# Kernel tuning notes

Measured on AMD Instinct MI355X. Metric: run time of the kernel, lower is better.

The kernel has to match this reference:

```python
import jax, jax.numpy as jnp
import numpy as np

B, S, E, D = 8, 2048, 512, 512  # batch, seq (mesh edges), elem_size, embd_size


def setup_inputs() -> dict:
    key = jax.random.key(0)
    ks = jax.random.split(key, 5)
    scale = 1.0 / np.sqrt(E)
    return {
        "x": jax.random.normal(ks[0], (B, S, E), dtype=jnp.float32),
        "Wq": jax.random.normal(ks[1], (E, D), dtype=jnp.float32) * scale,
        "bq": jax.random.normal(ks[2], (D,), dtype=jnp.float32) * 0.01,
        "Wk": jax.random.normal(ks[3], (E, D), dtype=jnp.float32) * scale,
        "bk": jax.random.normal(ks[4], (D,), dtype=jnp.float32) * 0.01,
    }


def reference(x, Wq, bq, Wk, bk):
    elem_size = x.shape[-1]
    q = jax.nn.relu(x @ Wq + bq)              # [B,S,D]
    k = jax.nn.relu(x @ Wk + bk)              # [B,S,D]
    scores = jnp.einsum("bqd,bkd->bqk", q, k) / (elem_size ** 0.5)  # [B,S,S]
    # nn.Softmax(dim=1): normalize over the QUERY axis (column-wise softmax)
    attn = jax.nn.softmax(scores, axis=1)
    new_values = jnp.einsum("bqk,bke->bqe", attn, x)  # V = raw x (use_V=False)
    return x + new_values                     # residual connection
```

## Files before the change

### kernel.cpp

```cpp
#include <hip/hip_runtime.h>
#include <hip/hip_bf16.h>
#include <math.h>

#define Bb 8
#define Ss 2048
#define Ee 512
#define Dd 512
#define QSPLIT 16

typedef __bf16 bf16x8 __attribute__((ext_vector_type(8)));
typedef __bf16 bf16x4 __attribute__((ext_vector_type(4)));
typedef float f32x4 __attribute__((ext_vector_type(4)));


__device__ __forceinline__ void stage64(ushort* lds, const __bf16* gbase,
                                        int ldg, int wave, int lane) {
#pragma unroll
    for (int t = 0; t < 4; ++t) {
        const int slot = wave * 256 + t * 64 + lane;
        const int row  = slot >> 3;
        const int c    = (slot & 7) ^ (row & 7);
        __builtin_amdgcn_global_load_lds(
            (const __attribute__((address_space(1))) void*)(gbase + (size_t)row * ldg + c * 8),
            (__attribute__((address_space(3))) void*)(lds + (size_t)slot * 8),
            16, 0, 0);
    }
}

__device__ __forceinline__ void stage64h(ushort* lds, const __bf16* gbase,
                                         int ldg, int wave, int lane) {
#pragma unroll
    for (int t = 0; t < 2; ++t) {
        const int slot = wave * 128 + t * 64 + lane;
        const int row  = slot >> 3;
        const int c    = (slot & 7) ^ (row & 7);
        __builtin_amdgcn_global_load_lds(
            (const __attribute__((address_space(1))) void*)(gbase + (size_t)row * ldg + c * 8),
            (__attribute__((address_space(3))) void*)(lds + (size_t)slot * 8),
            16, 0, 0);
    }
}

__global__ __launch_bounds__(256) void prep_x(const float* __restrict__ in,
                                              __bf16* __restrict__ xb,
                                              __bf16* __restrict__ xT) {
    __shared__ float tile[64][65];
    const int b  = blockIdx.z;
    const int e0 = blockIdx.x * 64;
    const int s0 = blockIdx.y * 64;
    const float* ip = in + (size_t)b * Ss * Ee;
    __bf16* xbp = xb + (size_t)b * Ss * Ee;
    __bf16* xTp = xT + (size_t)b * Ee * Ss;
    const int tid  = threadIdx.x;
    const int rrow = tid >> 4;
    const int c4   = (tid & 15) * 4;
    #pragma unroll
    for (int it = 0; it < 4; ++it) {
        const int r = it * 16 + rrow;
        const float4 v = *(const float4*)&ip[(size_t)(s0 + r) * Ee + e0 + c4];
        bf16x4 h;
        h[0] = (__bf16)v.x; h[1] = (__bf16)v.y; h[2] = (__bf16)v.z; h[3] = (__bf16)v.w;
        *(bf16x4*)&xbp[(size_t)(s0 + r) * Ee + e0 + c4] = h;
        tile[r][c4 + 0] = v.x; tile[r][c4 + 1] = v.y;
        tile[r][c4 + 2] = v.z; tile[r][c4 + 3] = v.w;
    }
    __syncthreads();
    const int sc  = (tid & 7) * 8;
    const int erb = tid >> 3;
    #pragma unroll
    for (int it = 0; it < 2; ++it) {
        const int er = it * 32 + erb;
        bf16x8 o;
        #pragma unroll
        for (int t = 0; t < 8; ++t) o[t] = (__bf16)tile[sc + t][er];
        *(bf16x8*)&xTp[(size_t)(e0 + er) * Ss + s0 + sc] = o;
    }
}

__global__ void transpose_w(const float* __restrict__ Wq, const float* __restrict__ Wk,
                            __bf16* __restrict__ WqT, __bf16* __restrict__ WkT) {
    __shared__ float tile[32][33];
    const float* in = blockIdx.z ? Wk : Wq;
    __bf16* out = blockIdx.z ? WkT : WqT;
    const int x0 = blockIdx.x * 32;
    const int y0 = blockIdx.y * 32;
    for (int i = threadIdx.y; i < 32; i += 8)
        tile[i][threadIdx.x] = in[(size_t)(y0 + i) * 512 + (x0 + threadIdx.x)];
    __syncthreads();
    for (int i = threadIdx.y; i < 32; i += 8)
        out[(size_t)(x0 + i) * 512 + (y0 + threadIdx.x)] = (__bf16)tile[threadIdx.x][i];
}

__global__ __launch_bounds__(256, 4) void proj_kernel(
    const __bf16* __restrict__ X,
    const __bf16* __restrict__ WqT, const __bf16* __restrict__ WkT,
    const float* __restrict__ bq, const float* __restrict__ bk,
    __bf16* __restrict__ qb, __bf16* __restrict__ kb)
{
    __shared__ __align__(16) ushort smem[2 * 128 * 64];
    ushort* As = smem;
    ushort* Bs = smem + 128 * 64;
    const __bf16* WT  = blockIdx.z ? WkT : WqT;
    const float* bias = blockIdx.z ? bk : bq;
    __bf16* Out       = blockIdx.z ? kb : qb;

    const int tid = threadIdx.x;
    const int wave = tid >> 6, lane = tid & 63, quad = lane >> 4, l16 = lane & 15;
    const int wm = (wave >> 1) * 64, wn = (wave & 1) * 64;
    const int m0 = blockIdx.y * 128, n0 = blockIdx.x * 128;
    const int K = 512;
    const int sw0 = ((quad)     ^ (l16 & 7)) * 8;
    const int sw1 = ((quad + 4) ^ (l16 & 7)) * 8;

    f32x4 acc[4][4];
    f32x4 zero = {0.f, 0.f, 0.f, 0.f};
    for (int i = 0; i < 4; i++) for (int j = 0; j < 4; j++) acc[i][j] = zero;

    for (int k0 = 0; k0 < K; k0 += 64) {
        stage64(As, X  + (size_t)m0 * K + k0, K, wave, lane);
        stage64(Bs, WT + (size_t)n0 * K + k0, K, wave, lane);
        __syncthreads();
        #pragma unroll
        for (int h = 0; h < 2; h++) {
            const int sw = h ? sw1 : sw0;
            bf16x8 af[4], bfr[4];
            for (int i = 0; i < 4; i++) af[i]  = *(bf16x8*)&As[(wm + i * 16 + l16) * 64 + sw];
            for (int j = 0; j < 4; j++) bfr[j] = *(bf16x8*)&Bs[(wn + j * 16 + l16) * 64 + sw];
            for (int i = 0; i < 4; i++)
                for (int j = 0; j < 4; j++)
                    acc[i][j] = __builtin_amdgcn_mfma_f32_16x16x32_bf16(af[i], bfr[j], acc[i][j], 0, 0, 0);
        }
        __syncthreads();
    }

    ushort* patch = smem + wave * 4096;
    for (int j = 0; j < 4; j++) {
        const float bv = bias[n0 + wn + j * 16 + l16];
        const int colsw = (j * 16 + l16) ^ (quad * 16);
        for (int i = 0; i < 4; i++)
            for (int rr = 0; rr < 4; rr++) {
                float v = acc[i][j][rr] + bv;
                v = v > 0.f ? v : 0.f;
                patch[(i * 16 + quad * 4 + rr) * 64 + colsw] = ((ushort2*)&v)[0].y;
            }
    }
    __syncthreads();
    #pragma unroll
    for (int it = 0; it < 8; it++) {
        const int lr = it * 8 + (lane >> 3);
        const int lc = ((lane & 7) * 8) ^ (((lr >> 2) & 3) * 16);
        const bf16x8 v = *(const bf16x8*)&patch[lr * 64 + lc];
        *(bf16x8*)&Out[(size_t)(m0 + wm + lr) * 512 + n0 + wn + (((lane & 7) * 8))] = v;
    }
}

__global__ __launch_bounds__(256, 4) void scores_kernel(
    const __bf16* __restrict__ Q,
    const __bf16* __restrict__ Km,
    __bf16* __restrict__ P,
    float* __restrict__ Lp)
{
    __shared__ __align__(16) ushort smem[2 * 128 * 64];
    __shared__ float stats[256];
    ushort* As = smem;
    ushort* Bs = smem + 128 * 64;
    const int id = blockIdx.x;
    const int b = id & 7;
    const int rest = id >> 3;
    const int qy = rest >> 4;
    const int m0 = qy * 128;
    const int n0 = (rest & 15) * 128;
    const __bf16* A  = Q  + (size_t)b * Ss * Dd;
    const __bf16* Bp = Km + (size_t)b * Ss * Dd;
    __bf16* C = P + (size_t)b * Ss * Ss;

    const int tid = threadIdx.x;
    const int wave = tid >> 6, lane = tid & 63, quad = lane >> 4, l16 = lane & 15;
    const int wm = (wave >> 1) * 64, wn = (wave & 1) * 64;
    const int sw0 = ((quad)     ^ (l16 & 7)) * 8;
    const int sw1 = ((quad + 4) ^ (l16 & 7)) * 8;
    const float scale = 0.044194173824159216f;
    const float SHIFT = 8.0f;

    f32x4 acc[4][4];
    f32x4 zero = {0.f, 0.f, 0.f, 0.f};
    for (int i = 0; i < 4; i++) for (int j = 0; j < 4; j++) acc[i][j] = zero;

    for (int k0 = 0; k0 < Dd; k0 += 64) {
        stage64(As, A  + (size_t)m0 * Dd + k0, Dd, wave, lane);
        stage64(Bs, Bp + (size_t)n0 * Dd + k0, Dd, wave, lane);
        __syncthreads();
        #pragma unroll
        for (int h = 0; h < 2; h++) {
            const int sw = h ? sw1 : sw0;
            bf16x8 af[4], bfr[4];
            for (int i = 0; i < 4; i++) af[i]  = *(bf16x8*)&As[(wm + i * 16 + l16) * 64 + sw];
            for (int j = 0; j < 4; j++) bfr[j] = *(bf16x8*)&Bs[(wn + j * 16 + l16) * 64 + sw];
            for (int i = 0; i < 4; i++)
                for (int j = 0; j < 4; j++)
                    acc[i][j] = __builtin_amdgcn_mfma_f32_16x16x32_bf16(af[i], bfr[j], acc[i][j], 0, 0, 0);
        }
        __syncthreads();
    }

    float* Ls = stats;
    const int half = wave >> 1;
    ushort* patch = smem + wave * 4096;
    float lj[4];
    for (int j = 0; j < 4; j++) {
        float l = 0.f;
        const int colsw = (j * 16 + l16) ^ (quad * 16);
        for (int i = 0; i < 4; i++)
            for (int rr = 0; rr < 4; rr++) {
                const float e = __expf(fmaf(acc[i][j][rr], scale, -SHIFT));
                const __bf16 pb = (__bf16)e;
                patch[(i * 16 + quad * 4 + rr) * 64 + colsw] = *(const ushort*)&pb;
                l += e;
            }
        l += __shfl_xor(l, 16);
        l += __shfl_xor(l, 32);
        lj[j] = l;
    }
    if (quad == 0)
        for (int j = 0; j < 4; j++) Ls[half * 128 + wn + j * 16 + l16] = lj[j];
    __syncthreads();
    if (tid < 128) {
        const size_t o = ((size_t)qy * Bb + b) * Ss + n0 + tid;
        Lp[o] = Ls[tid] + Ls[128 + tid];
    }
    #pragma unroll
    for (int it = 0; it < 8; it++) {
        const int lr = it * 8 + (lane >> 3);
        const int lc = ((lane & 7) * 8) ^ (((lr >> 2) & 3) * 16);
        const bf16x8 v = *(const bf16x8*)&patch[lr * 64 + lc];
        *(bf16x8*)&C[(size_t)(m0 + wm + lr) * Ss + n0 + wn + ((lane & 7) * 8)] = v;
    }
}

__global__ void stats_combine(const float* __restrict__ Lp, float* __restrict__ Cinv) {
    const int idx = blockIdx.x * 256 + threadIdx.x;
    float l = 0.f;
    for (int qy = 0; qy < QSPLIT; qy++) l += Lp[(size_t)qy * Bb * Ss + idx];
    Cinv[idx] = 1.0f / l;
}

__global__ void xscale_kernel(const __bf16* __restrict__ xT,
                              const float* __restrict__ Cinv,
                              __bf16* __restrict__ XC) {
    const int r = blockIdx.x;
    const int b = r >> 9;
    const size_t base = (size_t)r * Ss;
    const float* cp = Cinv + (size_t)b * Ss;
    const int k0 = threadIdx.x * 8;
    const bf16x8 v = *(const bf16x8*)&xT[base + k0];
    const float4 c0 = *(const float4*)&cp[k0];
    const float4 c1 = *(const float4*)&cp[k0 + 4];
    bf16x8 o;
    o[0] = (__bf16)((float)v[0] * c0.x);
    o[1] = (__bf16)((float)v[1] * c0.y);
    o[2] = (__bf16)((float)v[2] * c0.z);
    o[3] = (__bf16)((float)v[3] * c0.w);
    o[4] = (__bf16)((float)v[4] * c1.x);
    o[5] = (__bf16)((float)v[5] * c1.y);
    o[6] = (__bf16)((float)v[6] * c1.z);
    o[7] = (__bf16)((float)v[7] * c1.w);
    *(bf16x8*)&XC[base + k0] = o;
}

__global__ __launch_bounds__(256, 4) void pv_kernel(
    const __bf16* __restrict__ P,
    const __bf16* __restrict__ XC,
    const __bf16* __restrict__ XB,
    float* __restrict__ Out)
{
    __shared__ __align__(16) ushort smem[64 * 64 + 128 * 64];
    ushort* As = smem;
    ushort* Bs = smem + 64 * 64;
    const int id = blockIdx.x;
    const int b = id & 7;
    const int rest = id >> 3;
    const int m0 = (rest >> 2) * 64;
    const int n0 = (rest & 3) * 128;
    const __bf16* A  = P  + (size_t)b * Ss * Ss;
    const __bf16* Bp = XC + (size_t)b * Ee * Ss;

    const int tid = threadIdx.x;
    const int wave = tid >> 6, lane = tid & 63, quad = lane >> 4, l16 = lane & 15;
    const int wm = (wave >> 1) * 32, wn = (wave & 1) * 64;
    const int sw0 = ((quad)     ^ (l16 & 7)) * 8;
    const int sw1 = ((quad + 4) ^ (l16 & 7)) * 8;

    f32x4 acc[2][4];
    f32x4 zero = {0.f, 0.f, 0.f, 0.f};
    for (int i = 0; i < 2; i++) for (int j = 0; j < 4; j++) acc[i][j] = zero;

    for (int k0 = 0; k0 < Ss; k0 += 64) {
        stage64h(As, A  + (size_t)m0 * Ss + k0, Ss, wave, lane);
        stage64 (Bs, Bp + (size_t)n0 * Ss + k0, Ss, wave, lane);
        __syncthreads();
        #pragma unroll
        for (int h = 0; h < 2; h++) {
            const int sw = h ? sw1 : sw0;
            bf16x8 af[2], bfr[4];
            for (int i = 0; i < 2; i++) af[i]  = *(bf16x8*)&As[(wm + i * 16 + l16) * 64 + sw];
            for (int j = 0; j < 4; j++) bfr[j] = *(bf16x8*)&Bs[(wn + j * 16 + l16) * 64 + sw];
            for (int i = 0; i < 2; i++)
                for (int j = 0; j < 4; j++)
                    acc[i][j] = __builtin_amdgcn_mfma_f32_16x16x32_bf16(af[i], bfr[j], acc[i][j], 0, 0, 0);
        }
        __syncthreads();
    }

    for (int i = 0; i < 2; i++) {
        for (int j = 0; j < 4; j++) {
            const int col = n0 + wn + j * 16 + l16;
            for (int rr = 0; rr < 4; rr++) {
                const int row = m0 + wm + i * 16 + quad * 4 + rr;
                const size_t idx = ((size_t)b * Ss + row) * Ee + col;
                Out[idx] = (float)XB[idx] + acc[i][j][rr];
            }
        }
    }
}

extern "C" void kernel_launch(void* const* d_in, const int* in_sizes, int n_in,
                              void* d_out, int out_size, void* d_ws, size_t ws_size,
                              hipStream_t stream) {
    const float* x  = (const float*)d_in[0];
    const float* Wq = (const float*)d_in[1];
    const float* bq = (const float*)d_in[2];
    const float* Wk = (const float*)d_in[3];
    const float* bk = (const float*)d_in[4];
    float* out = (float*)d_out;

    char* ws = (char*)d_ws;
    size_t off = 0;
    auto alloc = [&](size_t bytes) -> void* {
        void* p = ws + off;
        off += (bytes + 255) & ~(size_t)255;
        return p;
    };
    __bf16* P    = (__bf16*)alloc((size_t)Bb * Ss * Ss * 2);
    __bf16* xb   = (__bf16*)alloc((size_t)Bb * Ss * Ee * 2);
    __bf16* qb   = (__bf16*)alloc((size_t)Bb * Ss * Dd * 2);
    __bf16* kb   = (__bf16*)alloc((size_t)Bb * Ss * Dd * 2);
    __bf16* xT   = (__bf16*)alloc((size_t)Bb * Ee * Ss * 2);
    __bf16* WqT  = (__bf16*)alloc((size_t)512 * 512 * 2);
    __bf16* WkT  = (__bf16*)alloc((size_t)512 * 512 * 2);
    float*  Lp   = (float*)alloc((size_t)QSPLIT * Bb * Ss * 4);
    float*  Cinv = (float*)alloc((size_t)Bb * Ss * 4);
    if (off > ws_size) return;
    __bf16* XC = qb;

    prep_x<<<dim3(8, 32, 8), 256, 0, stream>>>(x, xb, xT);
    transpose_w<<<dim3(16, 16, 2), dim3(32, 8), 0, stream>>>(Wq, Wk, WqT, WkT);

    proj_kernel<<<dim3(4, 128, 2), 256, 0, stream>>>(xb, WqT, WkT, bq, bk, qb, kb);

    scores_kernel<<<dim3(2048), 256, 0, stream>>>(qb, kb, P, Lp);
    stats_combine<<<dim3(Bb * Ss / 256), 256, 0, stream>>>(Lp, Cinv);

    xscale_kernel<<<dim3(Bb * Ee), 256, 0, stream>>>(xT, Cinv, XC);

    pv_kernel<<<dim3(1024), 256, 0, stream>>>(P, XC, xb, out);
}
```

Before: 221.7 us.

## Double-buffer LDS staging in proj, scores and pv GEMM kernels

Adds ping-pong LDS buffers to the three GEMM main loops. The next K-tile is prefetched with global_load_lds while the current one feeds the MFMAs, using explicit vmcnt waits and raw s_barrier in place of __syncthreads. The aim is to hide global-memory latency behind compute. In exchange, LDS per block doubles (64 KB for proj/scores), which may lower occupancy below the launch_bounds target of 4 blocks, and the hand-tuned vmcnt counts must match the number of loads each stage issues.

```diff
diff --git a/kernel.cpp b/kernel.cpp
--- a/kernel.cpp
+++ b/kernel.cpp
@@ -97,9 +97,11 @@
     const float* __restrict__ bq, const float* __restrict__ bk,
     __bf16* __restrict__ qb, __bf16* __restrict__ kb)
 {
-    __shared__ __align__(16) ushort smem[2 * 128 * 64];
-    ushort* As = smem;
-    ushort* Bs = smem + 128 * 64;
+    __shared__ __align__(16) ushort smem[4 * 128 * 64];
+    ushort* As0 = smem;
+    ushort* Bs0 = smem + 8192;
+    ushort* As1 = smem + 16384;
+    ushort* Bs1 = smem + 24576;
     const __bf16* WT  = blockIdx.z ? WkT : WqT;
     const float* bias = blockIdx.z ? bk : bq;
     __bf16* Out       = blockIdx.z ? kb : qb;
@@ -116,21 +118,35 @@
     f32x4 zero = {0.f, 0.f, 0.f, 0.f};
     for (int i = 0; i < 4; i++) for (int j = 0; j < 4; j++) acc[i][j] = zero;
 
-    for (int k0 = 0; k0 < K; k0 += 64) {
-        stage64(As, X  + (size_t)m0 * K + k0, K, wave, lane);
-        stage64(Bs, WT + (size_t)n0 * K + k0, K, wave, lane);
-        __syncthreads();
+    stage64(As0, X  + (size_t)m0 * K, K, wave, lane);
+    stage64(Bs0, WT + (size_t)n0 * K, K, wave, lane);
+    #pragma unroll
+    for (int t = 0; t < 8; ++t) {
+        ushort* Ac = (t & 1) ? As1 : As0;
+        ushort* Bc = (t & 1) ? Bs1 : Bs0;
+        if (t < 7) {
+            ushort* An = (t & 1) ? As0 : As1;
+            ushort* Bn = (t & 1) ? Bs0 : Bs1;
+            const int kn = (t + 1) * 64;
+            stage64(An, X  + (size_t)m0 * K + kn, K, wave, lane);
+            stage64(Bn, WT + (size_t)n0 * K + kn, K, wave, lane);
+            asm volatile("s_waitcnt vmcnt(8)" ::: "memory");
+        } else {
+            asm volatile("s_waitcnt vmcnt(0)" ::: "memory");
+        }
+        __builtin_amdgcn_s_barrier();
         #pragma unroll
         for (int h = 0; h < 2; h++) {
             const int sw = h ? sw1 : sw0;
             bf16x8 af[4], bfr[4];
-            for (int i = 0; i < 4; i++) af[i]  = *(bf16x8*)&As[(wm + i * 16 + l16) * 64 + sw];
-            for (int j = 0; j < 4; j++) bfr[j] = *(bf16x8*)&Bs[(wn + j * 16 + l16) * 64 + sw];
+            for (int i = 0; i < 4; i++) af[i]  = *(bf16x8*)&Ac[(wm + i * 16 + l16) * 64 + sw];
+            for (int j = 0; j < 4; j++) bfr[j] = *(bf16x8*)&Bc[(wn + j * 16 + l16) * 64 + sw];
             for (int i = 0; i < 4; i++)
                 for (int j = 0; j < 4; j++)
                     acc[i][j] = __builtin_amdgcn_mfma_f32_16x16x32_bf16(af[i], bfr[j], acc[i][j], 0, 0, 0);
         }
-        __syncthreads();
+        __builtin_amdgcn_sched_barrier(0);
+        __builtin_amdgcn_s_barrier();
     }
 
     ushort* patch = smem + wave * 4096;
@@ -160,10 +176,12 @@
     __bf16* __restrict__ P,
     float* __restrict__ Lp)
 {
-    __shared__ __align__(16) ushort smem[2 * 128 * 64];
+    __shared__ __align__(16) ushort smem[4 * 128 * 64];
     __shared__ float stats[256];
-    ushort* As = smem;
-    ushort* Bs = smem + 128 * 64;
+    ushort* As0 = smem;
+    ushort* Bs0 = smem + 8192;
+    ushort* As1 = smem + 16384;
+    ushort* Bs1 = smem + 24576;
     const int id = blockIdx.x;
     const int b = id & 7;
     const int rest = id >> 3;
@@ -186,21 +204,35 @@
     f32x4 zero = {0.f, 0.f, 0.f, 0.f};
     for (int i = 0; i < 4; i++) for (int j = 0; j < 4; j++) acc[i][j] = zero;
 
-    for (int k0 = 0; k0 < Dd; k0 += 64) {
-        stage64(As, A  + (size_t)m0 * Dd + k0, Dd, wave, lane);
-        stage64(Bs, Bp + (size_t)n0 * Dd + k0, Dd, wave, lane);
-        __syncthreads();
+    stage64(As0, A  + (size_t)m0 * Dd, Dd, wave, lane);
+    stage64(Bs0, Bp + (size_t)n0 * Dd, Dd, wave, lane);
+    #pragma unroll
+    for (int t = 0; t < 8; ++t) {
+        ushort* Ac = (t & 1) ? As1 : As0;
+        ushort* Bc = (t & 1) ? Bs1 : Bs0;
+        if (t < 7) {
+            ushort* An = (t & 1) ? As0 : As1;
+            ushort* Bn = (t & 1) ? Bs0 : Bs1;
+            const int kn = (t + 1) * 64;
+            stage64(An, A  + (size_t)m0 * Dd + kn, Dd, wave, lane);
+            stage64(Bn, Bp + (size_t)n0 * Dd + kn, Dd, wave, lane);
+            asm volatile("s_waitcnt vmcnt(8)" ::: "memory");
+        } else {
+            asm volatile("s_waitcnt vmcnt(0)" ::: "memory");
+        }
+        __builtin_amdgcn_s_barrier();
         #pragma unroll
         for (int h = 0; h < 2; h++) {
             const int sw = h ? sw1 : sw0;
             bf16x8 af[4], bfr[4];
-            for (int i = 0; i < 4; i++) af[i]  = *(bf16x8*)&As[(wm + i * 16 + l16) * 64 + sw];
-            for (int j = 0; j < 4; j++) bfr[j] = *(bf16x8*)&Bs[(wn + j * 16 + l16) * 64 + sw];
+            for (int i = 0; i < 4; i++) af[i]  = *(bf16x8*)&Ac[(wm + i * 16 + l16) * 64 + sw];
+            for (int j = 0; j < 4; j++) bfr[j] = *(bf16x8*)&Bc[(wn + j * 16 + l16) * 64 + sw];
             for (int i = 0; i < 4; i++)
                 for (int j = 0; j < 4; j++)
                     acc[i][j] = __builtin_amdgcn_mfma_f32_16x16x32_bf16(af[i], bfr[j], acc[i][j], 0, 0, 0);
         }
-        __syncthreads();
+        __builtin_amdgcn_sched_barrier(0);
+        __builtin_amdgcn_s_barrier();
     }
 
     float* Ls = stats;
@@ -273,9 +305,11 @@
     const __bf16* __restrict__ XB,
     float* __restrict__ Out)
 {
-    __shared__ __align__(16) ushort smem[64 * 64 + 128 * 64];
-    ushort* As = smem;
-    ushort* Bs = smem + 64 * 64;
+    __shared__ __align__(16) ushort smem[2 * (64 * 64 + 128 * 64)];
+    ushort* As0 = smem;
+    ushort* Bs0 = smem + 4096;
+    ushort* As1 = smem + 12288;
+    ushort* Bs1 = smem + 16384;
     const int id = blockIdx.x;
     const int b = id & 7;
     const int rest = id >> 3;
@@ -294,21 +328,35 @@
     f32x4 zero = {0.f, 0.f, 0.f, 0.f};
     for (int i = 0; i < 2; i++) for (int j = 0; j < 4; j++) acc[i][j] = zero;
 
-    for (int k0 = 0; k0 < Ss; k0 += 64) {
-        stage64h(As, A  + (size_t)m0 * Ss + k0, Ss, wave, lane);
-        stage64 (Bs, Bp + (size_t)n0 * Ss + k0, Ss, wave, lane);
-        __syncthreads();
+    stage64h(As0, A  + (size_t)m0 * Ss, Ss, wave, lane);
+    stage64 (Bs0, Bp + (size_t)n0 * Ss, Ss, wave, lane);
+    #pragma unroll 2
+    for (int t = 0; t < 32; ++t) {
+        ushort* Ac = (t & 1) ? As1 : As0;
+        ushort* Bc = (t & 1) ? Bs1 : Bs0;
+        if (t < 31) {
+            ushort* An = (t & 1) ? As0 : As1;
+            ushort* Bn = (t & 1) ? Bs0 : Bs1;
+            const int kn = (t + 1) * 64;
+            stage64h(An, A  + (size_t)m0 * Ss + kn, Ss, wave, lane);
+            stage64 (Bn, Bp + (size_t)n0 * Ss + kn, Ss, wave, lane);
+            asm volatile("s_waitcnt vmcnt(6)" ::: "memory");
+        } else {
+            asm volatile("s_waitcnt vmcnt(0)" ::: "memory");
+        }
+        __builtin_amdgcn_s_barrier();
         #pragma unroll
         for (int h = 0; h < 2; h++) {
             const int sw = h ? sw1 : sw0;
             bf16x8 af[2], bfr[4];
-            for (int i = 0; i < 2; i++) af[i]  = *(bf16x8*)&As[(wm + i * 16 + l16) * 64 + sw];
-            for (int j = 0; j < 4; j++) bfr[j] = *(bf16x8*)&Bs[(wn + j * 16 + l16) * 64 + sw];
+            for (int i = 0; i < 2; i++) af[i]  = *(bf16x8*)&Ac[(wm + i * 16 + l16) * 64 + sw];
+            for (int j = 0; j < 4; j++) bfr[j] = *(bf16x8*)&Bc[(wn + j * 16 + l16) * 64 + sw];
             for (int i = 0; i < 2; i++)
                 for (int j = 0; j < 4; j++)
                     acc[i][j] = __builtin_amdgcn_mfma_f32_16x16x32_bf16(af[i], bfr[j], acc[i][j], 0, 0, 0);
         }
-        __syncthreads();
+        __builtin_amdgcn_sched_barrier(0);
+        __builtin_amdgcn_s_barrier();
     }
 
     for (int i = 0; i < 2; i++) {
```

After: 211.6 us. 1.05x faster.
